# Kernel optimization log

Measured on AMD Instinct MI355X. Metric: run time of the kernel, lower is better.

The kernel has to match this reference:

```python
import jax, jax.numpy as jnp
import numpy as np

NH = 16   # neighbors
MD = 64   # model_dim
FF = 128  # ff_dim
H = 4     # heads
HD = MD // H
B, S, T = 2, 8192, 4096
LOG100 = float(np.log(100.0))


def _ln(x, g, b, eps=1e-5):
    m = x.mean(-1, keepdims=True)
    v = ((x - m) ** 2).mean(-1, keepdims=True)
    return (x - m) * jax.lax.rsqrt(v + eps) * g + b


def _lrelu(x):
    return jnp.where(x >= 0, x, 0.2 * x)


def setup_inputs():
    ks = jax.random.split(jax.random.key(0), 16)
    rn = lambda k, sh: jax.random.normal(k, sh, dtype=jnp.float32) * 0.05
    return {
        "x": jax.random.normal(ks[0], (B, S, 1), dtype=jnp.float32),
        "c1": jax.random.normal(ks[1], (B, S, T), dtype=jnp.float32),
        "c2": jax.random.normal(ks[2], (B, S, T), dtype=jnp.float32),
        "pe_W1": rn(ks[3], (2, FF)), "pe_b1": jnp.zeros((FF,), jnp.float32),
        "pe_W2": rn(ks[4], (FF, MD)), "pe_b2": jnp.zeros((MD,), jnp.float32),
        "Wq": rn(ks[5], (MD, MD)), "Wk": rn(ks[6], (MD, MD)), "Wv": rn(ks[7], (1, MD)),
        "logit_scale": jnp.full((H, 1, 1), float(np.log(10.0)), jnp.float32),
        "Wo": rn(ks[8], (MD, MD)), "bo": jnp.zeros((MD,), jnp.float32),
        "g1": jnp.ones((MD,), jnp.float32), "beta1": jnp.zeros((MD,), jnp.float32),
        "g2": jnp.ones((MD,), jnp.float32), "beta2": jnp.zeros((MD,), jnp.float32),
        "g3": jnp.ones((MD * NH,), jnp.float32), "beta3": jnp.zeros((MD * NH,), jnp.float32),
        "mnh_W1": rn(ks[9], (MD, FF)), "mnh_b1": jnp.zeros((FF,), jnp.float32),
        "mnh_W2": rn(ks[10], (FF, 1)), "mnh_b2": jnp.zeros((1,), jnp.float32),
        "mu_W1": rn(ks[11], (MD * NH, MD * NH)), "mu_b1": jnp.zeros((MD * NH,), jnp.float32),
        "mu_W2": rn(ks[12], (MD * NH, MD * NH)), "mu_b2": jnp.zeros((MD * NH,), jnp.float32),
    }


def reference(x, c1, c2, pe_W1, pe_b1, pe_W2, pe_b2, Wq, Wk, Wv, logit_scale, Wo, bo,
              g1, beta1, g2, beta2, g3, beta3,
              mnh_W1, mnh_b1, mnh_W2, mnh_b2, mu_W1, mu_b1, mu_W2, mu_b2):
    b, s, t = c1.shape
    # KNN over source axis s (cartesian distance), per target t
    d = c1 * c1 + c2 * c2                                  # [b,s,t]
    _, idx = jax.lax.top_k(-jnp.swapaxes(d, 1, 2), NH)     # [b,t,NH]
    x_nh = jax.vmap(lambda xb, ib: xb[ib])(x, idx)         # [b,t,NH,e]
    c1g = jnp.take_along_axis(jnp.swapaxes(c1, 1, 2), idx, axis=2)  # [b,t,NH]
    c2g = jnp.take_along_axis(jnp.swapaxes(c2, 1, 2), idx, axis=2)
    # relative-position embedding MLP (PE), already in [b,t,NH,MD] layout
    pe = jnp.stack([c1g, c2g], -1)                         # [b,t,NH,2]
    pe = jax.nn.gelu(pe @ pe_W1 + pe_b1) @ pe_W2 + pe_b2   # [b,t,NH,MD]
    h = _ln(x_nh + pe, g1, beta1).reshape(b * t, NH, MD)   # e=1 broadcasts
    v = jnp.einsum('bne,ed->bnd', x_nh.reshape(b * t, NH, 1), Wv)
    q = h @ Wq
    k = h @ Wk
    sp = lambda z: z.reshape(b * t, NH, H, HD).transpose(0, 2, 1, 3)
    qh, kh, vh = sp(q), sp(k), sp(v)
    # logit-scaled (cosine) attention over the NH neighbor axis
    qn = qh * jax.lax.rsqrt(jnp.sum(qh * qh, -1, keepdims=True) + 1e-12)
    kn = kh * jax.lax.rsqrt(jnp.sum(kh * kh, -1, keepdims=True) + 1e-12)
    scale = jnp.exp(jnp.minimum(logit_scale, LOG100))      # [H,1,1]
    att = jax.nn.softmax(jnp.einsum('bhnd,bhmd->bhnm', qn, kn) * scale, axis=-1)
    o = jnp.einsum('bhnm,bhmd->bhnd', att, vh).transpose(0, 2, 1, 3).reshape(b * t, NH, MD)
    h = _ln(h + (o @ Wo + bo), g2, beta2)
    # per-neighbor MLP producing a scalar, broadcast-added back
    h = h + _lrelu(_lrelu(h @ mnh_W1 + mnh_b1) @ mnh_W2 + mnh_b2)
    # unfold neighbors into channels and run the unfold MLP
    h = _ln(h.reshape(b, t, NH * MD), g3, beta3)
    return _lrelu(_lrelu(h @ mu_W1 + mu_b1) @ mu_W2 + mu_b2)  # [b,t,NH*MD]
```

## Files before the change

kernel.cpp:

```cpp
#include <hip/hip_runtime.h>
#include <hip/hip_bf16.h>

#define B_    2
#define SSRC  8192
#define TT    4096
#define NHN   16
#define NC    64
#define CS    128
#define LOG100D 4.605170185988091368035982909368

typedef short s16x8 __attribute__((ext_vector_type(8)));
typedef float f32x4 __attribute__((ext_vector_type(4)));
typedef double f64x4 __attribute__((ext_vector_type(4)));
typedef unsigned long long u64;

typedef const __attribute__((address_space(1))) void* gas_ptr;
typedef __attribute__((address_space(3))) void* las_ptr;
#define GLDS16(g, l) __builtin_amdgcn_global_load_lds((gas_ptr)(g), (las_ptr)(l), 16, 0, 0)

#define WFENCE asm volatile("s_waitcnt lgkmcnt(0)" ::: "memory")

__device__ __forceinline__ unsigned short f2bf(float f) {
    unsigned u = __float_as_uint(f);
    u = u + 0x7fffu + ((u >> 16) & 1u);
    return (unsigned short)(u >> 16);
}
__device__ __forceinline__ float bf2f(unsigned short h) {
    return __uint_as_float(((unsigned)h) << 16);
}
__device__ __forceinline__ double lrelu_d(double v) { return v >= 0.0 ? v : 0.2 * v; }
__device__ __forceinline__ double gelu_d(double u) {
    double a = 0.7978845608028654 * (u + 0.044715 * u * u * u);
    return 0.5 * u * (1.0 + tanh(a));
}
__device__ __forceinline__ double rsum16d(double v) {
    v += __shfl_xor(v, 1); v += __shfl_xor(v, 2);
    v += __shfl_xor(v, 4); v += __shfl_xor(v, 8);
    return v;
}
__device__ __forceinline__ double rmax16d(double v) {
    v = fmax(v, __shfl_xor(v, 1)); v = fmax(v, __shfl_xor(v, 2));
    v = fmax(v, __shfl_xor(v, 4)); v = fmax(v, __shfl_xor(v, 8));
    return v;
}
__device__ __forceinline__ double rsum64d(double v) {
    v += __shfl_xor(v, 1); v += __shfl_xor(v, 2); v += __shfl_xor(v, 4);
    v += __shfl_xor(v, 8); v += __shfl_xor(v, 16); v += __shfl_xor(v, 32);
    return v;
}

__device__ __forceinline__ int mfma64_discover() {
    int lane = threadIdx.x & 63;
    int l15 = lane & 15, lg = lane >> 4;
    double va = (double)(1 + ((lane * 37) % 61));
    double vb = (double)(2 + ((lane * 53) % 59));
    f64x4 d = (f64x4){0.0, 0.0, 0.0, 0.0};
    d = __builtin_amdgcn_mfma_f64_16x16x4f64(va, vb, d, 0, 0, 0);
    int found = -1;
#pragma unroll
    for (int c = 0; c < 8; c++) {
        int dm = (c >> 2) & 1, am = (c >> 1) & 1, bm = c & 1;
        bool ok = true;
#pragma unroll
        for (int r = 0; r < 4; r++) {
            int i = dm ? (lg + 4 * r) : (4 * lg + r);
            int j = l15;
            double e = 0.0;
#pragma unroll
            for (int k = 0; k < 4; k++) {
                int la = am ? (4 * i + k) : (i + 16 * k);
                int lb = bm ? (4 * j + k) : (j + 16 * k);
                e += (double)(1 + ((la * 37) % 61)) * (double)(2 + ((lb * 53) % 59));
            }
            ok = ok && (d[r] == e);
        }
        if (__all(ok) && found < 0) found = c;
    }
    return found;
}

__device__ __forceinline__ void ce(u64 &a, u64 &b) {
    bool c = a < b; u64 lo = c ? a : b; u64 hi = c ? b : a; a = lo; b = hi;
}
__device__ __forceinline__ void sort16(u64 (&k)[16]) {
    ce(k[0],k[8]); ce(k[1],k[9]); ce(k[2],k[10]); ce(k[3],k[11]);
    ce(k[4],k[12]); ce(k[5],k[13]); ce(k[6],k[14]); ce(k[7],k[15]);
    ce(k[0],k[4]); ce(k[1],k[5]); ce(k[2],k[6]); ce(k[3],k[7]);
    ce(k[8],k[12]); ce(k[9],k[13]); ce(k[10],k[14]); ce(k[11],k[15]);
    ce(k[4],k[8]); ce(k[5],k[9]); ce(k[6],k[10]); ce(k[7],k[11]);
    ce(k[0],k[2]); ce(k[1],k[3]); ce(k[4],k[6]); ce(k[5],k[7]);
    ce(k[8],k[10]); ce(k[9],k[11]); ce(k[12],k[14]); ce(k[13],k[15]);
    ce(k[2],k[8]); ce(k[3],k[9]); ce(k[6],k[12]); ce(k[7],k[13]);
    ce(k[2],k[4]); ce(k[3],k[5]); ce(k[6],k[8]); ce(k[7],k[9]);
    ce(k[10],k[12]); ce(k[11],k[13]);
    ce(k[0],k[1]); ce(k[2],k[3]); ce(k[4],k[5]); ce(k[6],k[7]);
    ce(k[8],k[9]); ce(k[10],k[11]); ce(k[12],k[13]); ce(k[14],k[15]);
    ce(k[1],k[8]); ce(k[3],k[10]); ce(k[5],k[12]); ce(k[7],k[14]);
    ce(k[1],k[4]); ce(k[3],k[6]); ce(k[5],k[8]); ce(k[7],k[10]);
    ce(k[9],k[12]); ce(k[11],k[14]);
    ce(k[1],k[2]); ce(k[3],k[4]); ce(k[5],k[6]); ce(k[7],k[8]);
    ce(k[9],k[10]); ce(k[11],k[12]); ce(k[13],k[14]);
}
__device__ __forceinline__ void bmerge16(u64 (&k)[16]) {
    ce(k[0],k[8]); ce(k[1],k[9]); ce(k[2],k[10]); ce(k[3],k[11]);
    ce(k[4],k[12]); ce(k[5],k[13]); ce(k[6],k[14]); ce(k[7],k[15]);
    ce(k[0],k[4]); ce(k[1],k[5]); ce(k[2],k[6]); ce(k[3],k[7]);
    ce(k[8],k[12]); ce(k[9],k[13]); ce(k[10],k[14]); ce(k[11],k[15]);
    ce(k[0],k[2]); ce(k[1],k[3]); ce(k[4],k[6]); ce(k[5],k[7]);
    ce(k[8],k[10]); ce(k[9],k[11]); ce(k[12],k[14]); ce(k[13],k[15]);
    ce(k[0],k[1]); ce(k[2],k[3]); ce(k[4],k[5]); ce(k[6],k[7]);
    ce(k[8],k[9]); ce(k[10],k[11]); ce(k[12],k[13]); ce(k[14],k[15]);
}
__device__ __forceinline__ void merge_keep16(u64 (&L)[16], const u64 (&B)[16]) {
#pragma unroll
    for (int i = 0; i < 16; i++) { u64 bb = B[15 - i]; L[i] = L[i] < bb ? L[i] : bb; }
    bmerge16(L);
}

__global__ __launch_bounds__(256) void topk_partial(
    const float* __restrict__ c1, const float* __restrict__ c2,
    u64* __restrict__ cand)
{
    int t = blockIdx.x * 256 + threadIdx.x;
    int ch = blockIdx.y, b = blockIdx.z;
    const float* p1 = c1 + ((size_t)b * SSRC + (size_t)ch * CS) * TT + t;
    const float* p2 = c2 + ((size_t)b * SSRC + (size_t)ch * CS) * TT + t;
    u64 k[16];
#pragma unroll
    for (int j = 0; j < 16; j++) k[j] = ~0ull;
    int sbase = ch * CS;
    for (int s = 0; s < CS; s += 16) {
        u64 bt[16];
#pragma unroll
        for (int u = 0; u < 16; u++) {
            float a_ = p1[(size_t)(s + u) * TT];
            float b_ = p2[(size_t)(s + u) * TT];
            float dd = __fadd_rn(__fmul_rn(a_, a_), __fmul_rn(b_, b_));
            bt[u] = ((u64)__float_as_uint(dd) << 32) | (unsigned)(sbase + s + u);
        }
        sort16(bt);
        merge_keep16(k, bt);
    }
    u64* dst = cand + ((size_t)(b * NC + ch) * 16) * TT + t;
#pragma unroll
    for (int j = 0; j < 16; j++) dst[(size_t)j * TT] = k[j];
}

__global__ __launch_bounds__(64) void topk_merge1(
    const u64* __restrict__ cand, u64* __restrict__ c2c)
{
    int t = blockIdx.x * 64 + threadIdx.x;
    int g = blockIdx.y, b = blockIdx.z;
    u64 k[16];
#pragma unroll
    for (int j = 0; j < 16; j++) k[j] = ~0ull;
    for (int c = g * 8; c < g * 8 + 8; c++) {
        const u64* src = cand + ((size_t)(b * NC + c) * 16) * TT + t;
        u64 bt[16];
#pragma unroll
        for (int j = 0; j < 16; j++) bt[j] = src[(size_t)j * TT];
        merge_keep16(k, bt);
    }
    u64* dst = c2c + ((size_t)((b * 8 + g) * 16)) * TT + t;
#pragma unroll
    for (int j = 0; j < 16; j++) dst[(size_t)j * TT] = k[j];
}

__global__ __launch_bounds__(64) void topk_merge2(
    const u64* __restrict__ c2c, int* __restrict__ knn)
{
    int t = blockIdx.x * 64 + threadIdx.x;
    int b = blockIdx.y;
    u64 k[16];
#pragma unroll
    for (int j = 0; j < 16; j++) k[j] = ~0ull;
    for (int c = 0; c < 8; c++) {
        const u64* src = c2c + ((size_t)(b * 8 + c) * 16) * TT + t;
        u64 bt[16];
#pragma unroll
        for (int j = 0; j < 16; j++) bt[j] = src[(size_t)j * TT];
        merge_keep16(k, bt);
    }
#pragma unroll
    for (int j = 0; j < 16; j++)
        knn[((size_t)b * TT + t) * 16 + j] = (int)(unsigned)(k[j] & 0xffffffffull);
}

__global__ __launch_bounds__(256) void wconv(
    const float* __restrict__ Wa, const float* __restrict__ Wb,
    unsigned short* __restrict__ Oah, unsigned short* __restrict__ Oal,
    unsigned short* __restrict__ Obh, unsigned short* __restrict__ Obl)
{
    const float* W = blockIdx.z ? Wb : Wa;
    unsigned short* Oh = blockIdx.z ? Obh : Oah;
    unsigned short* Ol = blockIdx.z ? Obl : Oal;
    __shared__ float tile[64][65];
    int tx = threadIdx.x & 63, ty = threadIdx.x >> 6;
    int n0 = blockIdx.x * 64, k0 = blockIdx.y * 64;
#pragma unroll
    for (int r = ty; r < 64; r += 4) tile[r][tx] = W[(size_t)(k0 + r) * 1024 + n0 + tx];
    __syncthreads();
#pragma unroll
    for (int r = ty; r < 64; r += 4) {
        float v = tile[tx][r];
        unsigned short hi = f2bf(v);
        Oh[(size_t)(n0 + r) * 1024 + k0 + tx] = hi;
        Ol[(size_t)(n0 + r) * 1024 + k0 + tx] = f2bf(v - bf2f(hi));
    }
}

__global__ __launch_bounds__(256) void tok_pe_m(
    const float* __restrict__ x, const float* __restrict__ c1, const float* __restrict__ c2,
    const int* __restrict__ knn,
    const float* __restrict__ peW1, const float* __restrict__ peb1,
    const float* __restrict__ peW2, const float* __restrict__ peb2,
    const float* __restrict__ g1, const float* __restrict__ be1,
    float* __restrict__ hout)
{
    int cand = mfma64_discover();
    if (cand < 0) return;
    __shared__ float s_peW1[256], s_peb1[128], s_peW2[8448], s_peb2[64], s_g1[64], s_be1[64];
    __shared__ float s_scr[4][2352];
    int tid = threadIdx.x, lane = tid & 63, w = tid >> 6;
    if (tid < 256) s_peW1[tid] = peW1[tid];
    if (tid < 128) s_peb1[tid] = peb1[tid];
    if (tid < 64) { s_peb2[tid] = peb2[tid]; s_g1[tid] = g1[tid]; s_be1[tid] = be1[tid]; }
    for (int i = tid; i < 8192; i += 256) s_peW2[(i >> 6) * 66 + (i & 63)] = peW2[i];
    __syncthreads();

    int l15 = lane & 15, lg = lane >> 4;
    int am = (cand >> 1) & 1, bm = cand & 1, dm = (cand >> 2) & 1;
    int a_i = am ? (lane >> 2) : l15;
    int a_k = am ? (lane & 3)  : lg;
    int b_k = bm ? (lane & 3)  : lg;
    int b_j = bm ? (lane >> 2) : l15;
    int i0 = dm ? lg : 4 * lg;
    int istep = dm ? 4 : 1;

    float* big = s_scr[w];
    float* sc1 = big + 2304; float* sc2 = big + 2320; float* sx = big + 2336;
    double w0a = s_peW1[lane], w1a = s_peW1[128 + lane], ba = s_peb1[lane];
    double w0b = s_peW1[64 + lane], w1b = s_peW1[192 + lane], bbv = s_peb1[64 + lane];
    double g1v[4], be1v[4], pb2v[4];
#pragma unroll
    for (int j = 0; j < 4; j++) {
        g1v[j]  = (double)s_g1[j * 16 + l15];
        be1v[j] = (double)s_be1[j * 16 + l15];
        pb2v[j] = (double)s_peb2[j * 16 + l15];
    }

    for (int it = 0; it < 4; ++it) {
        int tk = blockIdx.x * 16 + w * 4 + it;
        int bb = tk >> 12, tt = tk & (TT - 1);
        if (lane < 16) {
            int s = knn[(size_t)tk * 16 + lane];
            sc1[lane] = c1[((size_t)bb * SSRC + s) * TT + tt];
            sc2[lane] = c2[((size_t)bb * SSRC + s) * TT + tt];
            sx[lane]  = x[bb * SSRC + s];
        }
        WFENCE;
#pragma unroll
        for (int n = 0; n < 16; n++) {
            double a_ = (double)sc1[n], b_ = (double)sc2[n];
            big[lane * 18 + n]        = (float)gelu_d(a_ * w0a + b_ * w1a + ba);
            big[(lane + 64) * 18 + n] = (float)gelu_d(a_ * w0b + b_ * w1b + bbv);
        }
        WFENCE;
        f64x4 acc[4];
#pragma unroll
        for (int j = 0; j < 4; j++) acc[j] = (f64x4){0.0, 0.0, 0.0, 0.0};
        for (int ks = 0; ks < 32; ks++) {
            double a = (double)big[(4 * ks + a_k) * 18 + a_i];
            const float* wrow = &s_peW2[(4 * ks + b_k) * 66 + b_j];
#pragma unroll
            for (int j = 0; j < 4; j++)
                acc[j] = __builtin_amdgcn_mfma_f64_16x16x4f64(a, (double)wrow[j * 16], acc[j], 0, 0, 0);
        }
        float* op = hout + (size_t)tk * 1024;
#pragma unroll
        for (int r = 0; r < 4; r++) {
            int n = i0 + istep * r;
            double xr = (double)sx[n];
            double v[4], s = 0.0;
#pragma unroll
            for (int j = 0; j < 4; j++) { v[j] = acc[j][r] + pb2v[j] + xr; s += v[j]; }
            double m = rsum16d(s) * (1.0 / 64.0);
            double q = 0.0;
#pragma unroll
            for (int j = 0; j < 4; j++) { double d = v[j] - m; q += d * d; }
            double var = rsum16d(q) * (1.0 / 64.0);
            double rs = sqrt(var + 1e-5);
#pragma unroll
            for (int j = 0; j < 4; j++)
                op[n * 64 + j * 16 + l15] = (float)((v[j] - m) / rs * g1v[j] + be1v[j]);
        }
    }
}

__global__ __launch_bounds__(256) void tok_pe_v(
    const float* __restrict__ x, const float* __restrict__ c1, const float* __restrict__ c2,
    const int* __restrict__ knn,
    const float* __restrict__ peW1, const float* __restrict__ peb1,
    const float* __restrict__ peW2, const float* __restrict__ peb2,
    const float* __restrict__ g1, const float* __restrict__ be1,
    float* __restrict__ hout)
{
    int cand = mfma64_discover();
    if (cand >= 0) return;
    __shared__ float s_peW1[256], s_peb1[128], s_peW2[8448], s_peb2[64], s_g1[64], s_be1[64];
    __shared__ float s_scr[4][2352];
    int tid = threadIdx.x, lane = tid & 63, w = tid >> 6;
    if (tid < 256) s_peW1[tid] = peW1[tid];
    if (tid < 128) s_peb1[tid] = peb1[tid];
    if (tid < 64) { s_peb2[tid] = peb2[tid]; s_g1[tid] = g1[tid]; s_be1[tid] = be1[tid]; }
    for (int i = tid; i < 8192; i += 256) s_peW2[(i >> 6) * 66 + (i & 63)] = peW2[i];
    __syncthreads();

    float* big = s_scr[w];
    float* sc1 = big + 2304; float* sc2 = big + 2320; float* sx = big + 2336;
    double w0a = s_peW1[lane], w1a = s_peW1[128 + lane], ba = s_peb1[lane];
    double w0b = s_peW1[64 + lane], w1b = s_peW1[192 + lane], bbv = s_peb1[64 + lane];
    double gv = (double)s_g1[lane], bv = (double)s_be1[lane];
    double pb2 = (double)s_peb2[lane];

    for (int it = 0; it < 4; ++it) {
        int tk = blockIdx.x * 16 + w * 4 + it;
        int bb = tk >> 12, tt = tk & (TT - 1);
        if (lane < 16) {
            int s = knn[(size_t)tk * 16 + lane];
            sc1[lane] = c1[((size_t)bb * SSRC + s) * TT + tt];
            sc2[lane] = c2[((size_t)bb * SSRC + s) * TT + tt];
            sx[lane]  = x[bb * SSRC + s];
        }
        WFENCE;
#pragma unroll
        for (int n = 0; n < 16; n++) {
            double a_ = (double)sc1[n], b_ = (double)sc2[n];
            big[lane * 18 + n]        = (float)gelu_d(a_ * w0a + b_ * w1a + ba);
            big[(lane + 64) * 18 + n] = (float)gelu_d(a_ * w0b + b_ * w1b + bbv);
        }
        WFENCE;
        double acc[16];
#pragma unroll
        for (int n = 0; n < 16; n++) acc[n] = pb2;
        for (int f = 0; f < 128; f++) {
            double wv = (double)s_peW2[f * 66 + lane];
#pragma unroll
            for (int n = 0; n < 16; n += 2) {
                float2 gvv = *(const float2*)&big[f * 18 + n];
                acc[n]     += (double)gvv.x * wv;
                acc[n + 1] += (double)gvv.y * wv;
            }
        }
        float* op = hout + (size_t)tk * 1024 + lane;
#pragma unroll
        for (int n = 0; n < 16; n++) {
            double v = acc[n] + (double)sx[n];
            double m = rsum64d(v) * (1.0 / 64.0);
            double d = v - m;
            double var = rsum64d(d * d) * (1.0 / 64.0);
            op[n * 64] = (float)(d / sqrt(var + 1e-5) * gv + bv);
        }
    }
}

__global__ __launch_bounds__(256) void tok_attn_m(
    const float* __restrict__ x, const int* __restrict__ knn,
    const float* __restrict__ Wq, const float* __restrict__ Wk,
    const float* __restrict__ Wv, const float* __restrict__ lsc,
    const float* __restrict__ Wo, const float* __restrict__ bo,
    const float* __restrict__ g2, const float* __restrict__ be2,
    float* __restrict__ hio)
{
    int cand = mfma64_discover();
    if (cand < 0) return;
    __shared__ float s_Wq[4224], s_Wk[4224], s_WoV[256], s_bo[64], s_g2[64], s_be2[64];
    __shared__ float s_scr[4][2320];
    int tid = threadIdx.x, lane = tid & 63, w = tid >> 6;
    if (tid < 64) {
        s_bo[tid] = bo[tid]; s_g2[tid] = g2[tid]; s_be2[tid] = be2[tid];
        for (int hh = 0; hh < 4; hh++) {
            double a = 0.0;
            for (int hd = 0; hd < 16; hd++)
                a += (double)Wv[hh * 16 + hd] * (double)Wo[(hh * 16 + hd) * 64 + tid];
            s_WoV[hh * 64 + tid] = (float)a;
        }
    }
    for (int i = tid; i < 4096; i += 256) {
        s_Wq[(i >> 6) * 66 + (i & 63)] = Wq[i];
        s_Wk[(i >> 6) * 66 + (i & 63)] = Wk[i];
    }
    __syncthreads();

    int l15 = lane & 15, lg = lane >> 4;
    int am = (cand >> 1) & 1, bm = cand & 1, dm = (cand >> 2) & 1;
    int a_i = am ? (lane >> 2) : l15;
    int a_k = am ? (lane & 3)  : lg;
    int b_k = bm ? (lane & 3)  : lg;
    int b_j = bm ? (lane >> 2) : l15;
    int i0 = dm ? lg : 4 * lg;
    int istep = dm ? 4 : 1;

    int head = lg, mm = l15;
    double scaleh = exp(fmin((double)lsc[head], LOG100D));
    double wov0 = (double)s_WoV[lane], wov1 = (double)s_WoV[64 + lane];
    double wov2 = (double)s_WoV[128 + lane], wov3 = (double)s_WoV[192 + lane];
    double gv = (double)s_g2[lane], bv = (double)s_be2[lane], bov = (double)s_bo[lane];
    float* big = s_scr[w];
    float* sx = big + 2304;

    for (int it = 0; it < 4; ++it) {
        int tk = blockIdx.x * 16 + w * 4 + it;
        int bb = tk >> 12;
        if (lane < 16) {
            int s = knn[(size_t)tk * 16 + lane];
            sx[lane] = x[bb * SSRC + s];
        }
        float* hp = hio + (size_t)tk * 1024 + lane;
        double h[16];
#pragma unroll
        for (int n = 0; n < 16; n++) {
            h[n] = (double)hp[n * 64];
            big[lane * 18 + n] = (float)h[n];
        }
        WFENCE;
        f64x4 qa[4], ka[4];
#pragma unroll
        for (int j = 0; j < 4; j++) { qa[j] = (f64x4){0.,0.,0.,0.}; ka[j] = (f64x4){0.,0.,0.,0.}; }
        for (int ks = 0; ks < 16; ks++) {
            double a = (double)big[(4 * ks + a_k) * 18 + a_i];
            const float* wq = &s_Wq[(4 * ks + b_k) * 66 + b_j];
            const float* wk = &s_Wk[(4 * ks + b_k) * 66 + b_j];
#pragma unroll
            for (int j = 0; j < 4; j++) {
                qa[j] = __builtin_amdgcn_mfma_f64_16x16x4f64(a, (double)wq[j * 16], qa[j], 0, 0, 0);
                ka[j] = __builtin_amdgcn_mfma_f64_16x16x4f64(a, (double)wk[j * 16], ka[j], 0, 0, 0);
            }
        }
        WFENCE;
#pragma unroll
        for (int j = 0; j < 4; j++) {
#pragma unroll
            for (int r = 0; r < 4; r++) {
                double qq = qa[j][r], kk2 = ka[j][r];
                double sq = rsum16d(qq * qq);
                double sk = rsum16d(kk2 * kk2);
                qq  /= sqrt(sq + 1e-12);
                kk2 /= sqrt(sk + 1e-12);
                int n = i0 + istep * r;
                big[(j * 16 + l15) * 18 + n]        = (float)qq;
                big[1152 + (j * 16 + l15) * 18 + n] = (float)kk2;
            }
        }
        WFENCE;
        double A_[16];
        {
            double S[16];
#pragma unroll
            for (int n = 0; n < 16; n++) S[n] = 0.0;
            for (int hd = 0; hd < 16; hd++) {
                int r = head * 16 + hd;
                double kf = (double)big[1152 + r * 18 + mm];
#pragma unroll
                for (int n = 0; n < 16; n += 2) {
                    float2 qq = *(const float2*)&big[r * 18 + n];
                    S[n] += (double)qq.x * kf; S[n + 1] += (double)qq.y * kf;
                }
            }
            double xv = (double)sx[mm];
#pragma unroll
            for (int n = 0; n < 16; n++) {
                double sv = S[n] * scaleh;
                double mx = rmax16d(sv);
                double e = exp(sv - mx);
                double se = rsum16d(e);
                A_[n] = rsum16d((e / se) * xv);
            }
        }
#pragma unroll
        for (int n = 0; n < 16; n++) {
            double a0 = __shfl(A_[n], mm), a1 = __shfl(A_[n], 16 + mm);
            double a2 = __shfl(A_[n], 32 + mm), a3 = __shfl(A_[n], 48 + mm);
            double v = h[n] + a0 * wov0 + a1 * wov1 + a2 * wov2 + a3 * wov3 + bov;
            double m = rsum64d(v) * (1.0 / 64.0);
            double d = v - m;
            double var = rsum64d(d * d) * (1.0 / 64.0);
            hp[n * 64] = (float)(d / sqrt(var + 1e-5) * gv + bv);
        }
    }
}

__global__ __launch_bounds__(256) void tok_attn_v(
    const float* __restrict__ x, const int* __restrict__ knn,
    const float* __restrict__ Wq, const float* __restrict__ Wk,
    const float* __restrict__ Wv, const float* __restrict__ lsc,
    const float* __restrict__ Wo, const float* __restrict__ bo,
    const float* __restrict__ g2, const float* __restrict__ be2,
    float* __restrict__ hio)
{
    int cand = mfma64_discover();
    if (cand >= 0) return;
    __shared__ float s_Wq[4224], s_Wk[4224], s_WoV[256], s_bo[64], s_g2[64], s_be2[64];
    __shared__ float s_scr[4][2320];
    int tid = threadIdx.x, lane = tid & 63, w = tid >> 6;
    if (tid < 64) {
        s_bo[tid] = bo[tid]; s_g2[tid] = g2[tid]; s_be2[tid] = be2[tid];
        for (int hh = 0; hh < 4; hh++) {
            double a = 0.0;
            for (int hd = 0; hd < 16; hd++)
                a += (double)Wv[hh * 16 + hd] * (double)Wo[(hh * 16 + hd) * 64 + tid];
            s_WoV[hh * 64 + tid] = (float)a;
        }
    }
    for (int i = tid; i < 4096; i += 256) {
        s_Wq[(i >> 6) * 66 + (i & 63)] = Wq[i];
        s_Wk[(i >> 6) * 66 + (i & 63)] = Wk[i];
    }
    __syncthreads();

    int head = lane >> 4, mm = lane & 15;
    double scaleh = exp(fmin((double)lsc[head], LOG100D));
    double wov0 = (double)s_WoV[lane], wov1 = (double)s_WoV[64 + lane];
    double wov2 = (double)s_WoV[128 + lane], wov3 = (double)s_WoV[192 + lane];
    double gv = (double)s_g2[lane], bv = (double)s_be2[lane], bov = (double)s_bo[lane];
    float* big = s_scr[w];
    float* sx = big + 2304;

    for (int it = 0; it < 4; ++it) {
        int tk = blockIdx.x * 16 + w * 4 + it;
        int bb = tk >> 12;
        if (lane < 16) {
            int s = knn[(size_t)tk * 16 + lane];
            sx[lane] = x[bb * SSRC + s];
        }
        float* hp = hio + (size_t)tk * 1024 + lane;
        double h[16];
#pragma unroll
        for (int n = 0; n < 16; n++) {
            h[n] = (double)hp[n * 64];
            big[lane * 18 + n] = (float)h[n];
        }
        WFENCE;
        double q[16], k2[16];
#pragma unroll
        for (int n = 0; n < 16; n++) { q[n] = 0.0; k2[n] = 0.0; }
        for (int kk = 0; kk < 64; kk++) {
            double wq = (double)s_Wq[kk * 66 + lane], wk = (double)s_Wk[kk * 66 + lane];
#pragma unroll
            for (int n = 0; n < 16; n += 2) {
                float2 hv = *(const float2*)&big[kk * 18 + n];
                q[n]  += (double)hv.x * wq; q[n + 1]  += (double)hv.y * wq;
                k2[n] += (double)hv.x * wk; k2[n + 1] += (double)hv.y * wk;
            }
        }
#pragma unroll
        for (int n = 0; n < 16; n++) {
            double sq = rsum16d(q[n] * q[n]);   q[n]  /= sqrt(sq + 1e-12);
            double sk = rsum16d(k2[n] * k2[n]); k2[n] /= sqrt(sk + 1e-12);
        }
        WFENCE;
#pragma unroll
        for (int n = 0; n < 16; n++) {
            big[lane * 18 + n]        = (float)q[n];
            big[1152 + lane * 18 + n] = (float)k2[n];
        }
        WFENCE;
        double A_[16];
        {
            double S[16];
#pragma unroll
            for (int n = 0; n < 16; n++) S[n] = 0.0;
            for (int hd = 0; hd < 16; hd++) {
                int r = head * 16 + hd;
                double kf = (double)big[1152 + r * 18 + mm];
#pragma unroll
                for (int n = 0; n < 16; n += 2) {
                    float2 qq = *(const float2*)&big[r * 18 + n];
                    S[n] += (double)qq.x * kf; S[n + 1] += (double)qq.y * kf;
                }
            }
            double xv = (double)sx[mm];
#pragma unroll
            for (int n = 0; n < 16; n++) {
                double sv = S[n] * scaleh;
                double mx = rmax16d(sv);
                double e = exp(sv - mx);
                double se = rsum16d(e);
                A_[n] = rsum16d((e / se) * xv);
            }
        }
#pragma unroll
        for (int n = 0; n < 16; n++) {
            double a0 = __shfl(A_[n], mm), a1 = __shfl(A_[n], 16 + mm);
            double a2 = __shfl(A_[n], 32 + mm), a3 = __shfl(A_[n], 48 + mm);
            double v = h[n] + a0 * wov0 + a1 * wov1 + a2 * wov2 + a3 * wov3 + bov;
            double m = rsum64d(v) * (1.0 / 64.0);
            double d = v - m;
            double var = rsum64d(d * d) * (1.0 / 64.0);
            hp[n * 64] = (float)(d / sqrt(var + 1e-5) * gv + bv);
        }
    }
}

__global__ __launch_bounds__(256) void tok_mnh_m(
    const float* __restrict__ hin,
    const float* __restrict__ mW1, const float* __restrict__ mb1,
    const float* __restrict__ mW2, const float* __restrict__ mb2,
    const float* __restrict__ g3, const float* __restrict__ be3,
    unsigned short* __restrict__ hnh, unsigned short* __restrict__ hnl)
{
    int cand = mfma64_discover();
    if (cand < 0) return;
    __shared__ float s_mW1[8320], s_mb1[128], s_mW2[128], s_g3[1024], s_be3[1024];
    __shared__ float s_scr[4][1152];
    int tid = threadIdx.x, lane = tid & 63, w = tid >> 6;
    if (tid < 128) { s_mb1[tid] = mb1[tid]; s_mW2[tid] = mW2[tid]; }
    for (int i = tid; i < 8192; i += 256) s_mW1[(i >> 7) * 130 + (i & 127)] = mW1[i];
    for (int i = tid; i < 1024; i += 256) { s_g3[i] = g3[i]; s_be3[i] = be3[i]; }
    __syncthreads();

    int l15 = lane & 15, lg = lane >> 4;
    int am = (cand >> 1) & 1, bm = cand & 1, dm = (cand >> 2) & 1;
    int a_i = am ? (lane >> 2) : l15;
    int a_k = am ? (lane & 3)  : lg;
    int b_k = bm ? (lane & 3)  : lg;
    int b_j = bm ? (lane >> 2) : l15;
    int i0 = dm ? lg : 4 * lg;
    int istep = dm ? 4 : 1;

    double mb2s = (double)mb2[0];
    double mb1v[8], w2v[8];
#pragma unroll
    for (int j = 0; j < 8; j++) {
        mb1v[j] = (double)s_mb1[j * 16 + l15];
        w2v[j]  = (double)s_mW2[j * 16 + l15];
    }
    float* big = s_scr[w];

    for (int it = 0; it < 4; ++it) {
        int tk = blockIdx.x * 16 + w * 4 + it;
        const float* hp = hin + (size_t)tk * 1024 + lane;
        double h[16];
#pragma unroll
        for (int n = 0; n < 16; n++) {
            h[n] = (double)hp[n * 64];
            big[lane * 18 + n] = (float)h[n];
        }
        WFENCE;
        f64x4 acc[8];
#pragma unroll
        for (int j = 0; j < 8; j++) acc[j] = (f64x4){0.0, 0.0, 0.0, 0.0};
        for (int ks = 0; ks < 16; ks++) {
            double a = (double)big[(4 * ks + a_k) * 18 + a_i];
            const float* wrow = &s_mW1[(4 * ks + b_k) * 130 + b_j];
#pragma unroll
            for (int j = 0; j < 8; j++)
                acc[j] = __builtin_amdgcn_mfma_f64_16x16x4f64(a, (double)wrow[j * 16], acc[j], 0, 0, 0);
        }
        double p[4];
#pragma unroll
        for (int r = 0; r < 4; r++) {
            double s = 0.0;
#pragma unroll
            for (int j = 0; j < 8; j++) {
                double t = acc[j][r] + mb1v[j];
                s += lrelu_d(t) * w2v[j];
            }
            p[r] = rsum16d(s);
        }
        if (dm == 0) {
#pragma unroll
            for (int n = 0; n < 16; n++) {
                double pn = __shfl(p[n & 3], (n >> 2) * 16);
                h[n] += lrelu_d(pn + mb2s);
            }
        } else {
#pragma unroll
            for (int n = 0; n < 16; n++) {
                double pn = __shfl(p[n >> 2], (n & 3) * 16);
                h[n] += lrelu_d(pn + mb2s);
            }
        }
        double s1 = 0.0;
#pragma unroll
        for (int n = 0; n < 16; n++) s1 += h[n];
        s1 = rsum64d(s1) * (1.0 / 1024.0);
        double s2v = 0.0;
#pragma unroll
        for (int n = 0; n < 16; n++) { double d = h[n] - s1; s2v += d * d; }
        s2v = rsum64d(s2v) * (1.0 / 1024.0);
        double rs = 1.0 / sqrt(s2v + 1e-5);
        unsigned short* oph = hnh + (size_t)tk * 1024 + lane;
        unsigned short* opl = hnl + (size_t)tk * 1024 + lane;
#pragma unroll
        for (int n = 0; n < 16; n++) {
            double v = (h[n] - s1) * rs * (double)s_g3[n * 64 + lane] + (double)s_be3[n * 64 + lane];
            unsigned short hi = f2bf((float)v);
            oph[n * 64] = hi;
            opl[n * 64] = f2bf((float)(v - (double)bf2f(hi)));
        }
    }
}

__global__ __launch_bounds__(256) void tok_mnh_v(
    const float* __restrict__ hin,
    const float* __restrict__ mW1, const float* __restrict__ mb1,
    const float* __restrict__ mW2, const float* __restrict__ mb2,
    const float* __restrict__ g3, const float* __restrict__ be3,
    unsigned short* __restrict__ hnh, unsigned short* __restrict__ hnl)
{
    int cand = mfma64_discover();
    if (cand >= 0) return;
    __shared__ float s_mW1[8320], s_mb1[128], s_mW2[128], s_g3[1024], s_be3[1024];
    __shared__ float s_scr[4][1152];
    int tid = threadIdx.x, lane = tid & 63, w = tid >> 6;
    if (tid < 128) { s_mb1[tid] = mb1[tid]; s_mW2[tid] = mW2[tid]; }
    for (int i = tid; i < 8192; i += 256) s_mW1[(i >> 7) * 130 + (i & 127)] = mW1[i];
    for (int i = tid; i < 1024; i += 256) { s_g3[i] = g3[i]; s_be3[i] = be3[i]; }
    __syncthreads();

    double mb2s = (double)mb2[0];
    double mb1a = (double)s_mb1[lane], mb1b = (double)s_mb1[64 + lane];
    double w2a = (double)s_mW2[lane], w2b = (double)s_mW2[64 + lane];
    float* big = s_scr[w];

    for (int it = 0; it < 4; ++it) {
        int tk = blockIdx.x * 16 + w * 4 + it;
        const float* hp = hin + (size_t)tk * 1024 + lane;
        double h[16];
#pragma unroll
        for (int n = 0; n < 16; n++) {
            h[n] = (double)hp[n * 64];
            big[lane * 18 + n] = (float)h[n];
        }
        WFENCE;
        double t1a[16], t1b[16];
#pragma unroll
        for (int n = 0; n < 16; n++) { t1a[n] = mb1a; t1b[n] = mb1b; }
        for (int kk = 0; kk < 64; kk++) {
            double wa = (double)s_mW1[kk * 130 + lane], wb = (double)s_mW1[kk * 130 + 64 + lane];
#pragma unroll
            for (int n = 0; n < 16; n += 2) {
                float2 hv = *(const float2*)&big[kk * 18 + n];
                t1a[n] += (double)hv.x * wa; t1a[n + 1] += (double)hv.y * wa;
                t1b[n] += (double)hv.x * wb; t1b[n + 1] += (double)hv.y * wb;
            }
        }
#pragma unroll
        for (int n = 0; n < 16; n++) {
            double p = lrelu_d(t1a[n]) * w2a + lrelu_d(t1b[n]) * w2b;
            p = rsum64d(p);
            h[n] += lrelu_d(p + mb2s);
        }
        double s1 = 0.0;
#pragma unroll
        for (int n = 0; n < 16; n++) s1 += h[n];
        s1 = rsum64d(s1) * (1.0 / 1024.0);
        double s2v = 0.0;
#pragma unroll
        for (int n = 0; n < 16; n++) { double d = h[n] - s1; s2v += d * d; }
        s2v = rsum64d(s2v) * (1.0 / 1024.0);
        double rs = 1.0 / sqrt(s2v + 1e-5);
        unsigned short* oph = hnh + (size_t)tk * 1024 + lane;
        unsigned short* opl = hnl + (size_t)tk * 1024 + lane;
#pragma unroll
        for (int n = 0; n < 16; n++) {
            double v = (h[n] - s1) * rs * (double)s_g3[n * 64 + lane] + (double)s_be3[n * 64 + lane];
            unsigned short hi = f2bf((float)v);
            oph[n * 64] = hi;
            opl[n * 64] = f2bf((float)(v - (double)bf2f(hi)));
        }
    }
}

#define AH_OFF 0
#define AL_OFF 4096
#define BH_OFF 8192
#define BL_OFF 12288
template<int OUTSPLIT>
__global__ __launch_bounds__(256) void gemm_split(
    const unsigned short* __restrict__ Ah, const unsigned short* __restrict__ Al,
    const unsigned short* __restrict__ Bh, const unsigned short* __restrict__ Bl,
    const float* __restrict__ bias,
    unsigned short* __restrict__ oh, unsigned short* __restrict__ ol,
    float* __restrict__ of, int M, int N, int K)
{
    __shared__ unsigned short SM[16384];
    int tid = threadIdx.x, lane = tid & 63, w = tid >> 6;
    int wm = w >> 1, wn = w & 1;
    int m0 = blockIdx.y * 128, n0 = blockIdx.x * 128;
    f32x4 acc[4][4];
#pragma unroll
    for (int i = 0; i < 4; i++)
#pragma unroll
        for (int j = 0; j < 4; j++) acc[i][j] = (f32x4){0.f, 0.f, 0.f, 0.f};
    int row = tid >> 2, c8 = (tid & 3) * 8;
    size_t aoff = (size_t)(m0 + row) * K + c8;
    size_t boff = (size_t)(n0 + row) * K + c8;
    for (int kk = 0; kk < K; kk += 32) {
        __syncthreads();
        GLDS16(Ah + aoff + kk,                   SM + AH_OFF + tid * 8);
        GLDS16(Ah + aoff + (size_t)64 * K + kk,  SM + AH_OFF + 2048 + tid * 8);
        GLDS16(Al + aoff + kk,                   SM + AL_OFF + tid * 8);
        GLDS16(Al + aoff + (size_t)64 * K + kk,  SM + AL_OFF + 2048 + tid * 8);
        GLDS16(Bh + boff + kk,                   SM + BH_OFF + tid * 8);
        GLDS16(Bh + boff + (size_t)64 * K + kk,  SM + BH_OFF + 2048 + tid * 8);
        GLDS16(Bl + boff + kk,                   SM + BL_OFF + tid * 8);
        GLDS16(Bl + boff + (size_t)64 * K + kk,  SM + BL_OFF + 2048 + tid * 8);
        asm volatile("s_waitcnt vmcnt(0)" ::: "memory");
        __syncthreads();
        int kh = (lane >> 4) * 8, rA = wm * 64 + (lane & 15), rB = wn * 64 + (lane & 15);
        s16x8 afh[4], afl[4], bfh[4], bfl[4];
#pragma unroll
        for (int i = 0; i < 4; i++) {
            afh[i] = *(const s16x8*)&SM[AH_OFF + (rA + i * 16) * 32 + kh];
            afl[i] = *(const s16x8*)&SM[AL_OFF + (rA + i * 16) * 32 + kh];
            bfh[i] = *(const s16x8*)&SM[BH_OFF + (rB + i * 16) * 32 + kh];
            bfl[i] = *(const s16x8*)&SM[BL_OFF + (rB + i * 16) * 32 + kh];
        }
#pragma unroll
        for (int i = 0; i < 4; i++)
#pragma unroll
            for (int j = 0; j < 4; j++) {
                acc[i][j] = __builtin_amdgcn_mfma_f32_16x16x32_bf16(afl[i], bfh[j], acc[i][j], 0, 0, 0);
                acc[i][j] = __builtin_amdgcn_mfma_f32_16x16x32_bf16(afh[i], bfl[j], acc[i][j], 0, 0, 0);
                acc[i][j] = __builtin_amdgcn_mfma_f32_16x16x32_bf16(afh[i], bfh[j], acc[i][j], 0, 0, 0);
            }
    }
    float bc[4];
#pragma unroll
    for (int j = 0; j < 4; j++) bc[j] = bias[n0 + wn * 64 + j * 16 + (lane & 15)];
#pragma unroll
    for (int i = 0; i < 4; i++) {
#pragma unroll
        for (int j = 0; j < 4; j++) {
#pragma unroll
            for (int r = 0; r < 4; r++) {
                int rw = m0 + wm * 64 + i * 16 + (lane >> 4) * 4 + r;
                int cl = n0 + wn * 64 + j * 16 + (lane & 15);
                float v = acc[i][j][r] + bc[j];
                v = v >= 0.f ? v : 0.2f * v;
                if (OUTSPLIT) {
                    unsigned short hi = f2bf(v);
                    oh[(size_t)rw * N + cl] = hi;
                    ol[(size_t)rw * N + cl] = f2bf(v - bf2f(hi));
                } else {
                    of[(size_t)rw * N + cl] = v;
                }
            }
        }
    }
}

extern "C" void kernel_launch(void* const* d_in, const int* in_sizes, int n_in,
                              void* d_out, int out_size, void* d_ws, size_t ws_size,
                              hipStream_t stream)
{
    const float* x    = (const float*)d_in[0];
    const float* c1   = (const float*)d_in[1];
    const float* c2   = (const float*)d_in[2];
    const float* peW1 = (const float*)d_in[3];
    const float* peb1 = (const float*)d_in[4];
    const float* peW2 = (const float*)d_in[5];
    const float* peb2 = (const float*)d_in[6];
    const float* Wq   = (const float*)d_in[7];
    const float* Wk   = (const float*)d_in[8];
    const float* Wv   = (const float*)d_in[9];
    const float* lsc  = (const float*)d_in[10];
    const float* Wo   = (const float*)d_in[11];
    const float* bo   = (const float*)d_in[12];
    const float* g1   = (const float*)d_in[13];
    const float* be1  = (const float*)d_in[14];
    const float* g2   = (const float*)d_in[15];
    const float* be2  = (const float*)d_in[16];
    const float* g3   = (const float*)d_in[17];
    const float* be3  = (const float*)d_in[18];
    const float* mW1  = (const float*)d_in[19];
    const float* mb1  = (const float*)d_in[20];
    const float* mW2  = (const float*)d_in[21];
    const float* mb2  = (const float*)d_in[22];
    const float* muW1 = (const float*)d_in[23];
    const float* mub1 = (const float*)d_in[24];
    const float* muW2 = (const float*)d_in[25];
    const float* mub2 = (const float*)d_in[26];

    const size_t MB = (size_t)1 << 20;
    char* ws = (char*)d_ws;
    u64*            cand   = (u64*)(ws);
    float*          hbuf   = (float*)(ws);
    unsigned short* y1h    = (unsigned short*)(ws);
    unsigned short* y1l    = (unsigned short*)(ws + 16 * MB);
    unsigned short* hnh    = (unsigned short*)(ws + 32 * MB);
    unsigned short* hnl    = (unsigned short*)(ws + 48 * MB);
    u64*            c2c    = (u64*)(ws + 64 * MB);
    unsigned short* w1th   = (unsigned short*)(ws + 72 * MB);
    unsigned short* w1tl   = (unsigned short*)(ws + 74 * MB);
    unsigned short* w2th   = (unsigned short*)(ws + 76 * MB);
    unsigned short* w2tl   = (unsigned short*)(ws + 78 * MB);
    int*            knn    = (int*)(ws + 80 * MB);
    (void)in_sizes; (void)n_in; (void)out_size; (void)ws_size;

    wconv<<<dim3(16, 16, 2), 256, 0, stream>>>(muW1, muW2, w1th, w1tl, w2th, w2tl);
    topk_partial<<<dim3(TT / 256, NC, B_), 256, 0, stream>>>(c1, c2, cand);
    topk_merge1<<<dim3(TT / 64, 8, B_), 64, 0, stream>>>(cand, c2c);
    topk_merge2<<<dim3(TT / 64, B_), 64, 0, stream>>>(c2c, knn);
    tok_pe_m<<<dim3(512), 256, 0, stream>>>(x, c1, c2, knn, peW1, peb1, peW2, peb2, g1, be1, hbuf);
    tok_pe_v<<<dim3(512), 256, 0, stream>>>(x, c1, c2, knn, peW1, peb1, peW2, peb2, g1, be1, hbuf);
    tok_attn_m<<<dim3(512), 256, 0, stream>>>(x, knn, Wq, Wk, Wv, lsc, Wo, bo, g2, be2, hbuf);
    tok_attn_v<<<dim3(512), 256, 0, stream>>>(x, knn, Wq, Wk, Wv, lsc, Wo, bo, g2, be2, hbuf);
    tok_mnh_m<<<dim3(512), 256, 0, stream>>>(hbuf, mW1, mb1, mW2, mb2, g3, be3, hnh, hnl);
    tok_mnh_v<<<dim3(512), 256, 0, stream>>>(hbuf, mW1, mb1, mW2, mb2, g3, be3, hnh, hnl);
    gemm_split<1><<<dim3(8, 64), 256, 0, stream>>>(hnh, hnl, w1th, w1tl, mub1,
                                                   y1h, y1l, (float*)nullptr, 8192, 1024, 1024);
    gemm_split<0><<<dim3(8, 64), 256, 0, stream>>>(y1h, y1l, w2th, w2tl, mub2,
                                                   (unsigned short*)nullptr, (unsigned short*)nullptr,
                                                   (float*)d_out, 8192, 1024, 1024);
}
```

Baseline: 816.6 us.

## Read small weights from global instead of LDS, and drop the attention MFMA variant

Removes the per-block staging of peW2, Wq/Wk and mnh_W1 into shared memory, so each kernel reads these weights straight from global memory (served by cache). This cuts LDS footprint and the block-startup copy, which could raise occupancy. It also merges the attention kernel's MFMA and vector variants into a single vector-FMA kernel, dropping the MFMA discovery step and one launch. In exchange, the inner loops now issue global loads per iteration, and the attention projection loses its f64 MFMA path.

```diff
diff --git a/kernel.cpp b/kernel.cpp
--- a/kernel.cpp
+++ b/kernel.cpp
@@ -219,13 +219,12 @@
 {
     int cand = mfma64_discover();
     if (cand < 0) return;
-    __shared__ float s_peW1[256], s_peb1[128], s_peW2[8448], s_peb2[64], s_g1[64], s_be1[64];
+    __shared__ float s_peW1[256], s_peb1[128], s_peb2[64], s_g1[64], s_be1[64];
     __shared__ float s_scr[4][2352];
     int tid = threadIdx.x, lane = tid & 63, w = tid >> 6;
     if (tid < 256) s_peW1[tid] = peW1[tid];
     if (tid < 128) s_peb1[tid] = peb1[tid];
     if (tid < 64) { s_peb2[tid] = peb2[tid]; s_g1[tid] = g1[tid]; s_be1[tid] = be1[tid]; }
-    for (int i = tid; i < 8192; i += 256) s_peW2[(i >> 6) * 66 + (i & 63)] = peW2[i];
     __syncthreads();
 
     int l15 = lane & 15, lg = lane >> 4;
@@ -271,7 +270,7 @@
         for (int j = 0; j < 4; j++) acc[j] = (f64x4){0.0, 0.0, 0.0, 0.0};
         for (int ks = 0; ks < 32; ks++) {
             double a = (double)big[(4 * ks + a_k) * 18 + a_i];
-            const float* wrow = &s_peW2[(4 * ks + b_k) * 66 + b_j];
+            const float* wrow = peW2 + (4 * ks + b_k) * 64 + b_j;
 #pragma unroll
             for (int j = 0; j < 4; j++)
                 acc[j] = __builtin_amdgcn_mfma_f64_16x16x4f64(a, (double)wrow[j * 16], acc[j], 0, 0, 0);
@@ -307,13 +306,12 @@
 {
     int cand = mfma64_discover();
     if (cand >= 0) return;
-    __shared__ float s_peW1[256], s_peb1[128], s_peW2[8448], s_peb2[64], s_g1[64], s_be1[64];
+    __shared__ float s_peW1[256], s_peb1[128], s_peb2[64], s_g1[64], s_be1[64];
     __shared__ float s_scr[4][2352];
     int tid = threadIdx.x, lane = tid & 63, w = tid >> 6;
     if (tid < 256) s_peW1[tid] = peW1[tid];
     if (tid < 128) s_peb1[tid] = peb1[tid];
     if (tid < 64) { s_peb2[tid] = peb2[tid]; s_g1[tid] = g1[tid]; s_be1[tid] = be1[tid]; }
-    for (int i = tid; i < 8192; i += 256) s_peW2[(i >> 6) * 66 + (i & 63)] = peW2[i];
     __syncthreads();
 
     float* big = s_scr[w];
@@ -344,7 +342,7 @@
 #pragma unroll
         for (int n = 0; n < 16; n++) acc[n] = pb2;
         for (int f = 0; f < 128; f++) {
-            double wv = (double)s_peW2[f * 66 + lane];
+            double wv = (double)peW2[f * 64 + lane];
 #pragma unroll
             for (int n = 0; n < 16; n += 2) {
                 float2 gvv = *(const float2*)&big[f * 18 + n];
@@ -364,7 +362,7 @@
     }
 }
 
-__global__ __launch_bounds__(256) void tok_attn_m(
+__global__ __launch_bounds__(256) void tok_attn(
     const float* __restrict__ x, const int* __restrict__ knn,
     const float* __restrict__ Wq, const float* __restrict__ Wk,
     const float* __restrict__ Wv, const float* __restrict__ lsc,
@@ -372,9 +370,7 @@
     const float* __restrict__ g2, const float* __restrict__ be2,
     float* __restrict__ hio)
 {
-    int cand = mfma64_discover();
-    if (cand < 0) return;
-    __shared__ float s_Wq[4224], s_Wk[4224], s_WoV[256], s_bo[64], s_g2[64], s_be2[64];
+    __shared__ float s_WoV[256], s_bo[64], s_g2[64], s_be2[64];
     __shared__ float s_scr[4][2320];
     int tid = threadIdx.x, lane = tid & 63, w = tid >> 6;
     if (tid < 64) {
@@ -386,22 +382,9 @@
             s_WoV[hh * 64 + tid] = (float)a;
         }
     }
-    for (int i = tid; i < 4096; i += 256) {
-        s_Wq[(i >> 6) * 66 + (i & 63)] = Wq[i];
-        s_Wk[(i >> 6) * 66 + (i & 63)] = Wk[i];
-    }
     __syncthreads();
 
-    int l15 = lane & 15, lg = lane >> 4;
-    int am = (cand >> 1) & 1, bm = cand & 1, dm = (cand >> 2) & 1;
-    int a_i = am ? (lane >> 2) : l15;
-    int a_k = am ? (lane & 3)  : lg;
-    int b_k = bm ? (lane & 3)  : lg;
-    int b_j = bm ? (lane >> 2) : l15;
-    int i0 = dm ? lg : 4 * lg;
-    int istep = dm ? 4 : 1;
-
-    int head = lg, mm = l15;
+    int head = lane >> 4, mm = lane & 15;
     double scaleh = exp(fmin((double)lsc[head], LOG100D));
     double wov0 = (double)s_WoV[lane], wov1 = (double)s_WoV[64 + lane];
     double wov2 = (double)s_WoV[128 + lane], wov3 = (double)s_WoV[192 + lane];
@@ -424,33 +407,28 @@
             big[lane * 18 + n] = (float)h[n];
         }
         WFENCE;
-        f64x4 qa[4], ka[4];
-#pragma unroll
-        for (int j = 0; j < 4; j++) { qa[j] = (f64x4){0.,0.,0.,0.}; ka[j] = (f64x4){0.,0.,0.,0.}; }
-        for (int ks = 0; ks < 16; ks++) {
-            double a = (double)big[(4 * ks + a_k) * 18 + a_i];
-            const float* wq = &s_Wq[(4 * ks + b_k) * 66 + b_j];
-            const float* wk = &s_Wk[(4 * ks + b_k) * 66 + b_j];
-#pragma unroll
-            for (int j = 0; j < 4; j++) {
-                qa[j] = __builtin_amdgcn_mfma_f64_16x16x4f64(a, (double)wq[j * 16], qa[j], 0, 0, 0);
-                ka[j] = __builtin_amdgcn_mfma_f64_16x16x4f64(a, (double)wk[j * 16], ka[j], 0, 0, 0);
-            }
-        }
-        WFENCE;
-#pragma unroll
-        for (int j = 0; j < 4; j++) {
-#pragma unroll
-            for (int r = 0; r < 4; r++) {
-                double qq = qa[j][r], kk2 = ka[j][r];
-                double sq = rsum16d(qq * qq);
-                double sk = rsum16d(kk2 * kk2);
-                qq  /= sqrt(sq + 1e-12);
-                kk2 /= sqrt(sk + 1e-12);
-                int n = i0 + istep * r;
-                big[(j * 16 + l15) * 18 + n]        = (float)qq;
-                big[1152 + (j * 16 + l15) * 18 + n] = (float)kk2;
-            }
+        double q[16], k2[16];
+#pragma unroll
+        for (int n = 0; n < 16; n++) { q[n] = 0.0; k2[n] = 0.0; }
+        for (int kk = 0; kk < 64; kk++) {
+            double wq = (double)Wq[kk * 64 + lane], wk = (double)Wk[kk * 64 + lane];
+#pragma unroll
+            for (int n = 0; n < 16; n += 2) {
+                float2 hv = *(const float2*)&big[kk * 18 + n];
+                q[n]  += (double)hv.x * wq; q[n + 1]  += (double)hv.y * wq;
+                k2[n] += (double)hv.x * wk; k2[n + 1] += (double)hv.y * wk;
+            }
+        }
+#pragma unroll
+        for (int n = 0; n < 16; n++) {
+            double sq = rsum16d(q[n] * q[n]);   q[n]  /= sqrt(sq + 1e-12);
+            double sk = rsum16d(k2[n] * k2[n]); k2[n] /= sqrt(sk + 1e-12);
+        }
+        WFENCE;
+#pragma unroll
+        for (int n = 0; n < 16; n++) {
+            big[lane * 18 + n]        = (float)q[n];
+            big[1152 + lane * 18 + n] = (float)k2[n];
         }
         WFENCE;
         double A_[16];
@@ -490,118 +468,6 @@
     }
 }
 
-__global__ __launch_bounds__(256) void tok_attn_v(
-    const float* __restrict__ x, const int* __restrict__ knn,
-    const float* __restrict__ Wq, const float* __restrict__ Wk,
-    const float* __restrict__ Wv, const float* __restrict__ lsc,
-    const float* __restrict__ Wo, const float* __restrict__ bo,
-    const float* __restrict__ g2, const float* __restrict__ be2,
-    float* __restrict__ hio)
-{
-    int cand = mfma64_discover();
-    if (cand >= 0) return;
-    __shared__ float s_Wq[4224], s_Wk[4224], s_WoV[256], s_bo[64], s_g2[64], s_be2[64];
-    __shared__ float s_scr[4][2320];
-    int tid = threadIdx.x, lane = tid & 63, w = tid >> 6;
-    if (tid < 64) {
-        s_bo[tid] = bo[tid]; s_g2[tid] = g2[tid]; s_be2[tid] = be2[tid];
-        for (int hh = 0; hh < 4; hh++) {
-            double a = 0.0;
-            for (int hd = 0; hd < 16; hd++)
-                a += (double)Wv[hh * 16 + hd] * (double)Wo[(hh * 16 + hd) * 64 + tid];
-            s_WoV[hh * 64 + tid] = (float)a;
-        }
-    }
-    for (int i = tid; i < 4096; i += 256) {
-        s_Wq[(i >> 6) * 66 + (i & 63)] = Wq[i];
-        s_Wk[(i >> 6) * 66 + (i & 63)] = Wk[i];
-    }
-    __syncthreads();
-
-    int head = lane >> 4, mm = lane & 15;
-    double scaleh = exp(fmin((double)lsc[head], LOG100D));
-    double wov0 = (double)s_WoV[lane], wov1 = (double)s_WoV[64 + lane];
-    double wov2 = (double)s_WoV[128 + lane], wov3 = (double)s_WoV[192 + lane];
-    double gv = (double)s_g2[lane], bv = (double)s_be2[lane], bov = (double)s_bo[lane];
-    float* big = s_scr[w];
-    float* sx = big + 2304;
-
-    for (int it = 0; it < 4; ++it) {
-        int tk = blockIdx.x * 16 + w * 4 + it;
-        int bb = tk >> 12;
-        if (lane < 16) {
-            int s = knn[(size_t)tk * 16 + lane];
-            sx[lane] = x[bb * SSRC + s];
-        }
-        float* hp = hio + (size_t)tk * 1024 + lane;
-        double h[16];
-#pragma unroll
-        for (int n = 0; n < 16; n++) {
-            h[n] = (double)hp[n * 64];
-            big[lane * 18 + n] = (float)h[n];
-        }
-        WFENCE;
-        double q[16], k2[16];
-#pragma unroll
-        for (int n = 0; n < 16; n++) { q[n] = 0.0; k2[n] = 0.0; }
-        for (int kk = 0; kk < 64; kk++) {
-            double wq = (double)s_Wq[kk * 66 + lane], wk = (double)s_Wk[kk * 66 + lane];
-#pragma unroll
-            for (int n = 0; n < 16; n += 2) {
-                float2 hv = *(const float2*)&big[kk * 18 + n];
-                q[n]  += (double)hv.x * wq; q[n + 1]  += (double)hv.y * wq;
-                k2[n] += (double)hv.x * wk; k2[n + 1] += (double)hv.y * wk;
-            }
-        }
-#pragma unroll
-        for (int n = 0; n < 16; n++) {
-            double sq = rsum16d(q[n] * q[n]);   q[n]  /= sqrt(sq + 1e-12);
-            double sk = rsum16d(k2[n] * k2[n]); k2[n] /= sqrt(sk + 1e-12);
-        }
-        WFENCE;
-#pragma unroll
-        for (int n = 0; n < 16; n++) {
-            big[lane * 18 + n]        = (float)q[n];
-            big[1152 + lane * 18 + n] = (float)k2[n];
-        }
-        WFENCE;
-        double A_[16];
-        {
-            double S[16];
-#pragma unroll
-            for (int n = 0; n < 16; n++) S[n] = 0.0;
-            for (int hd = 0; hd < 16; hd++) {
-                int r = head * 16 + hd;
-                double kf = (double)big[1152 + r * 18 + mm];
-#pragma unroll
-                for (int n = 0; n < 16; n += 2) {
-                    float2 qq = *(const float2*)&big[r * 18 + n];
-                    S[n] += (double)qq.x * kf; S[n + 1] += (double)qq.y * kf;
-                }
-            }
-            double xv = (double)sx[mm];
-#pragma unroll
-            for (int n = 0; n < 16; n++) {
-                double sv = S[n] * scaleh;
-                double mx = rmax16d(sv);
-                double e = exp(sv - mx);
-                double se = rsum16d(e);
-                A_[n] = rsum16d((e / se) * xv);
-            }
-        }
-#pragma unroll
-        for (int n = 0; n < 16; n++) {
-            double a0 = __shfl(A_[n], mm), a1 = __shfl(A_[n], 16 + mm);
-            double a2 = __shfl(A_[n], 32 + mm), a3 = __shfl(A_[n], 48 + mm);
-            double v = h[n] + a0 * wov0 + a1 * wov1 + a2 * wov2 + a3 * wov3 + bov;
-            double m = rsum64d(v) * (1.0 / 64.0);
-            double d = v - m;
-            double var = rsum64d(d * d) * (1.0 / 64.0);
-            hp[n * 64] = (float)(d / sqrt(var + 1e-5) * gv + bv);
-        }
-    }
-}
-
 __global__ __launch_bounds__(256) void tok_mnh_m(
     const float* __restrict__ hin,
     const float* __restrict__ mW1, const float* __restrict__ mb1,
@@ -611,11 +477,10 @@
 {
     int cand = mfma64_discover();
     if (cand < 0) return;
-    __shared__ float s_mW1[8320], s_mb1[128], s_mW2[128], s_g3[1024], s_be3[1024];
+    __shared__ float s_mb1[128], s_mW2[128], s_g3[1024], s_be3[1024];
     __shared__ float s_scr[4][1152];
     int tid = threadIdx.x, lane = tid & 63, w = tid >> 6;
     if (tid < 128) { s_mb1[tid] = mb1[tid]; s_mW2[tid] = mW2[tid]; }
-    for (int i = tid; i < 8192; i += 256) s_mW1[(i >> 7) * 130 + (i & 127)] = mW1[i];
     for (int i = tid; i < 1024; i += 256) { s_g3[i] = g3[i]; s_be3[i] = be3[i]; }
     __syncthreads();
 
@@ -625,8 +490,6 @@
     int a_k = am ? (lane & 3)  : lg;
     int b_k = bm ? (lane & 3)  : lg;
     int b_j = bm ? (lane >> 2) : l15;
-    int i0 = dm ? lg : 4 * lg;
-    int istep = dm ? 4 : 1;
 
     double mb2s = (double)mb2[0];
     double mb1v[8], w2v[8];
@@ -652,7 +515,7 @@
         for (int j = 0; j < 8; j++) acc[j] = (f64x4){0.0, 0.0, 0.0, 0.0};
         for (int ks = 0; ks < 16; ks++) {
             double a = (double)big[(4 * ks + a_k) * 18 + a_i];
-            const float* wrow = &s_mW1[(4 * ks + b_k) * 130 + b_j];
+            const float* wrow = mW1 + (4 * ks + b_k) * 128 + b_j;
 #pragma unroll
             for (int j = 0; j < 8; j++)
                 acc[j] = __builtin_amdgcn_mfma_f64_16x16x4f64(a, (double)wrow[j * 16], acc[j], 0, 0, 0);
@@ -711,11 +574,10 @@
 {
     int cand = mfma64_discover();
     if (cand >= 0) return;
-    __shared__ float s_mW1[8320], s_mb1[128], s_mW2[128], s_g3[1024], s_be3[1024];
+    __shared__ float s_mb1[128], s_mW2[128], s_g3[1024], s_be3[1024];
     __shared__ float s_scr[4][1152];
     int tid = threadIdx.x, lane = tid & 63, w = tid >> 6;
     if (tid < 128) { s_mb1[tid] = mb1[tid]; s_mW2[tid] = mW2[tid]; }
-    for (int i = tid; i < 8192; i += 256) s_mW1[(i >> 7) * 130 + (i & 127)] = mW1[i];
     for (int i = tid; i < 1024; i += 256) { s_g3[i] = g3[i]; s_be3[i] = be3[i]; }
     __syncthreads();
 
@@ -738,7 +600,7 @@
 #pragma unroll
         for (int n = 0; n < 16; n++) { t1a[n] = mb1a; t1b[n] = mb1b; }
         for (int kk = 0; kk < 64; kk++) {
-            double wa = (double)s_mW1[kk * 130 + lane], wb = (double)s_mW1[kk * 130 + 64 + lane];
+            double wa = (double)mW1[kk * 128 + lane], wb = (double)mW1[kk * 128 + 64 + lane];
 #pragma unroll
             for (int n = 0; n < 16; n += 2) {
                 float2 hv = *(const float2*)&big[kk * 18 + n];
@@ -906,8 +768,7 @@
     topk_merge2<<<dim3(TT / 64, B_), 64, 0, stream>>>(c2c, knn);
     tok_pe_m<<<dim3(512), 256, 0, stream>>>(x, c1, c2, knn, peW1, peb1, peW2, peb2, g1, be1, hbuf);
     tok_pe_v<<<dim3(512), 256, 0, stream>>>(x, c1, c2, knn, peW1, peb1, peW2, peb2, g1, be1, hbuf);
-    tok_attn_m<<<dim3(512), 256, 0, stream>>>(x, knn, Wq, Wk, Wv, lsc, Wo, bo, g2, be2, hbuf);
-    tok_attn_v<<<dim3(512), 256, 0, stream>>>(x, knn, Wq, Wk, Wv, lsc, Wo, bo, g2, be2, hbuf);
+    tok_attn<<<dim3(512), 256, 0, stream>>>(x, knn, Wq, Wk, Wv, lsc, Wo, bo, g2, be2, hbuf);
     tok_mnh_m<<<dim3(512), 256, 0, stream>>>(hbuf, mW1, mb1, mW2, mb2, g3, be3, hnh, hnl);
     tok_mnh_v<<<dim3(512), 256, 0, stream>>>(hbuf, mW1, mb1, mW2, mb2, g3, be3, hnh, hnl);
     gemm_split<1><<<dim3(8, 64), 256, 0, stream>>>(hnh, hnl, w1th, w1tl, mub1,
```

Result: slower. 896.3 us (+9.8%).
